# Kernel tuning notes

Measured on AMD Instinct MI355X. Metric: run time of the kernel, lower is better.

Reference implementation:

```python
import jax, jax.numpy as jnp
import numpy as np
import math

BS, LQ, LKV = 4, 2048, 2048
D_LATENT, D_MODEL, HEADS = 512, 512, 8
D_K = D_MODEL // HEADS


def setup_inputs() -> dict:
    key = jax.random.key(0)
    ks = jax.random.split(key, 12)
    s = 0.02
    return {
        "q": jax.random.normal(ks[0], (BS, LQ, D_LATENT), jnp.float32),
        "k": jax.random.normal(ks[1], (BS, LKV, D_MODEL), jnp.float32),
        "v": jax.random.normal(ks[2], (BS, LKV, D_MODEL), jnp.float32),
        "weights": jax.random.uniform(ks[3], (BS, LKV), jnp.float32) + 1e-3,
        "Wq": jax.random.normal(ks[4], (D_LATENT, D_MODEL), jnp.float32) * s,
        "bq": jnp.zeros((D_MODEL,), jnp.float32),
        "Wk": jax.random.normal(ks[5], (D_MODEL, D_MODEL), jnp.float32) * s,
        "bk": jnp.zeros((D_MODEL,), jnp.float32),
        "Wv": jax.random.normal(ks[6], (D_MODEL, D_MODEL), jnp.float32) * s,
        "bv": jnp.zeros((D_MODEL,), jnp.float32),
        "Wo": jax.random.normal(ks[7], (D_MODEL, D_MODEL), jnp.float32) * s,
        "bo": jnp.zeros((D_MODEL,), jnp.float32),
    }


def reference(q, k, v, weights, Wq, bq, Wk, bk, Wv, bv, Wo, bo):
    bs = q.shape[0]
    # QKV projections, split into heads: [bs, h, L, d_k]
    qh = (q @ Wq + bq).reshape(bs, -1, HEADS, D_K).transpose(0, 2, 1, 3)
    kh = (k @ Wk + bk).reshape(bs, -1, HEADS, D_K).transpose(0, 2, 1, 3)
    vh = (v @ Wv + bv).reshape(bs, -1, HEADS, D_K).transpose(0, 2, 1, 3)
    # scaled dot-product scores [bs, h, Lq, Lkv]
    scores = jnp.einsum("bhqd,bhkd->bhqk", qh, kh) / math.sqrt(D_K)
    p = jax.nn.softmax(scores, axis=-1)
    # post-softmax external weight renormalization
    wp = p * weights[:, None, None, :]
    wp = wp / wp.sum(-1, keepdims=True)
    out = jnp.einsum("bhqk,bhkd->bhqd", wp, vh)
    concat = out.transpose(0, 2, 1, 3).reshape(bs, -1, D_MODEL)
    return concat @ Wo + bo
```

## Files before the change

### kernel.cpp

```cpp
#include <hip/hip_runtime.h>
#include <hip/hip_bf16.h>

#define LQ 2048
#define LKV 2048
#define DM 512
#define NH 8
#define DK 64

typedef __attribute__((ext_vector_type(8))) __bf16 bf16x8;
typedef __attribute__((ext_vector_type(4))) float f32x4;
typedef __attribute__((ext_vector_type(16))) float f32x16;

#define AS1 __attribute__((address_space(1)))
#define AS3 __attribute__((address_space(3)))

static __device__ __forceinline__ unsigned short f2bf(float x) {
  unsigned u = __float_as_uint(x);
  return (unsigned short)((u + 0x7fffu + ((u >> 16) & 1u)) >> 16);
}
static __device__ __forceinline__ float bf2f(unsigned short u) {
  return __uint_as_float(((unsigned)u) << 16);
}
static __device__ __forceinline__ bf16x8 cvt8(f32x4 a, f32x4 b) {
  bf16x8 r;
  r[0] = (__bf16)a[0]; r[1] = (__bf16)a[1]; r[2] = (__bf16)a[2]; r[3] = (__bf16)a[3];
  r[4] = (__bf16)b[0]; r[5] = (__bf16)b[1]; r[6] = (__bf16)b[2]; r[7] = (__bf16)b[3];
  return r;
}

__global__ __launch_bounds__(256) void transpose_w(
    const float* __restrict__ Wq, const float* __restrict__ Wk,
    const float* __restrict__ Wv, const float* __restrict__ Wo,
    const float* __restrict__ wts,
    unsigned short* __restrict__ WtAll, unsigned short* __restrict__ wbf)
{
  const float* W = blockIdx.z == 0 ? Wq : blockIdx.z == 1 ? Wk : blockIdx.z == 2 ? Wv : Wo;
  unsigned short* Wt = WtAll + (size_t)blockIdx.z * DM * DM;
  __shared__ float tile[32][33];
  const int t = threadIdx.x;
  if (blockIdx.z == 0 && blockIdx.y == 0) {
    int idx = blockIdx.x * 512 + t * 2;
#pragma unroll
    for (int i = 0; i < 2; ++i) {
      int kv = idx + i;
      int r = kv & 15;
      int ph = (r & 3) | ((r & 4) << 1) | ((r & 8) >> 1);
      wbf[(kv & ~15) | ph] = f2bf(wts[kv]);
    }
  }
  const int tr = t >> 3;
  const int tc4 = (t & 7) * 4;
  const int k0 = blockIdx.x * 32, n0 = blockIdx.y * 32;
  float4 v = *(const float4*)(W + (size_t)(k0 + tr) * DM + n0 + tc4);
  tile[tr][tc4 + 0] = v.x; tile[tr][tc4 + 1] = v.y;
  tile[tr][tc4 + 2] = v.z; tile[tr][tc4 + 3] = v.w;
  __syncthreads();
  ushort4 o;
  o.x = f2bf(tile[tc4 + 0][tr]);
  o.y = f2bf(tile[tc4 + 1][tr]);
  o.z = f2bf(tile[tc4 + 2][tr]);
  o.w = f2bf(tile[tc4 + 3][tr]);
  *(ushort4*)(Wt + (size_t)(n0 + tr) * DM + k0 + tc4) = o;
}

__global__ __launch_bounds__(256) void gemm_qkv(
    const float* __restrict__ qin, const float* __restrict__ kin, const float* __restrict__ vin,
    const unsigned short* __restrict__ WtAll,
    const float* __restrict__ bq, const float* __restrict__ bk, const float* __restrict__ bv,
    unsigned short* __restrict__ qh, unsigned short* __restrict__ kh, unsigned short* __restrict__ vh)
{
  const int bid = blockIdx.x;
  const int x = bid & 7, j = bid >> 3;
  const int p = x + 8 * (j >> 2);
  const int nt = j & 3;
  const int mode = p >> 6, mtile = p & 63;

  const float* A = mode == 0 ? qin : (mode == 1 ? kin : vin);
  const unsigned short* Bt = WtAll + (size_t)mode * DM * DM;
  const float* bias = mode == 0 ? bq : (mode == 1 ? bk : bv);
  unsigned short* out = mode == 0 ? qh : (mode == 1 ? kh : vh);
  const float scale = (mode == 0) ? 0.18033688011112042f : 1.0f;

  __shared__ __align__(16) float As[128 * 32];
  __shared__ __align__(16) unsigned short Bs[128 * 32];

  const int tid = threadIdx.x;
  const int lane = tid & 63;
  const int w = tid >> 6;
  const int wr = w >> 1, wc = w & 1;
  const int l15 = lane & 15, g = lane >> 4;
  const int m0 = mtile * 128, n0 = nt * 128;

  f32x4 acc[4][4] = {};

  for (int k0 = 0; k0 < DM; k0 += 32) {
#pragma unroll
    for (int i = 0; i < 4; ++i) {
      int c = tid + i * 256;
      int row = c >> 3, slot = c & 7;
      const float* src = A + (size_t)(m0 + row) * DM + k0 + ((slot ^ (row & 7)) << 2);
      __builtin_amdgcn_global_load_lds((const AS1 unsigned*)src,
                                       (AS3 unsigned*)((char*)As + c * 16), 16, 0, 0);
    }
#pragma unroll
    for (int i = 0; i < 2; ++i) {
      int c = tid + i * 256;
      int row = c >> 2, slot = c & 3;
      const unsigned short* src = Bt + (size_t)(n0 + row) * DM + k0 + ((slot ^ ((row >> 1) & 3)) * 8);
      __builtin_amdgcn_global_load_lds((const AS1 unsigned*)src,
                                       (AS3 unsigned*)((char*)Bs + c * 16), 16, 0, 0);
    }
    __syncthreads();

    bf16x8 af[4], bfr[4];
#pragma unroll
    for (int mi = 0; mi < 4; ++mi) {
      int row = wr * 64 + mi * 16 + l15;
      f32x4 a0 = *(const f32x4*)((const char*)As + row * 128 + (((2 * g) ^ (row & 7)) << 4));
      f32x4 a1 = *(const f32x4*)((const char*)As + row * 128 + (((2 * g + 1) ^ (row & 7)) << 4));
      af[mi] = cvt8(a0, a1);
    }
#pragma unroll
    for (int ni = 0; ni < 4; ++ni) {
      int row = wc * 64 + ni * 16 + l15;
      bfr[ni] = *(const bf16x8*)((const char*)Bs + row * 64 + ((g ^ ((row >> 1) & 3)) * 16));
    }
#pragma unroll
    for (int mi = 0; mi < 4; ++mi)
#pragma unroll
      for (int ni = 0; ni < 4; ++ni)
        acc[mi][ni] = __builtin_amdgcn_mfma_f32_16x16x32_bf16(af[mi], bfr[ni], acc[mi][ni], 0, 0, 0);
    __syncthreads();
  }

#pragma unroll
  for (int mi = 0; mi < 4; ++mi) {
#pragma unroll
    for (int ni = 0; ni < 4; ++ni) {
      int n = n0 + wc * 64 + ni * 16 + l15;
      float bs = bias[n];
      int h = n >> 6, d = n & 63;
#pragma unroll
      for (int r = 0; r < 4; ++r) {
        int m = m0 + wr * 64 + mi * 16 + g * 4 + r;
        int b = m >> 11, li = m & 2047;
        float val = (acc[mi][ni][r] + bs) * scale;
        out[(((size_t)(b * NH + h)) * LQ + li) * DK + d] = f2bf(val);
      }
    }
  }
}

__global__ __launch_bounds__(256) void gemm_out(
    const unsigned short* __restrict__ A, const unsigned short* __restrict__ Bt,
    const float* __restrict__ bias, float* __restrict__ out)
{
  __shared__ __align__(16) unsigned short Al[128 * 32];
  __shared__ __align__(16) unsigned short Bl[128 * 32];
  const int tid = threadIdx.x;
  const int lane = tid & 63;
  const int w = tid >> 6;
  const int wr = w >> 1, wc = w & 1;
  const int l15 = lane & 15, g = lane >> 4;
  const int m0 = blockIdx.x * 128, n0 = blockIdx.y * 128;
  f32x4 acc[4][4] = {};

  for (int k0 = 0; k0 < DM; k0 += 32) {
#pragma unroll
    for (int i = 0; i < 2; ++i) {
      int c = tid + i * 256;
      int row = c >> 2, slot = c & 3;
      int so = (slot ^ ((row >> 1) & 3)) * 8;
      __builtin_amdgcn_global_load_lds(
          (const AS1 unsigned*)(A + (size_t)(m0 + row) * DM + k0 + so),
          (AS3 unsigned*)((char*)Al + c * 16), 16, 0, 0);
      __builtin_amdgcn_global_load_lds(
          (const AS1 unsigned*)(Bt + (size_t)(n0 + row) * DM + k0 + so),
          (AS3 unsigned*)((char*)Bl + c * 16), 16, 0, 0);
    }
    __syncthreads();
    bf16x8 af[4], bfr[4];
#pragma unroll
    for (int mi = 0; mi < 4; ++mi) {
      int row = wr * 64 + mi * 16 + l15;
      af[mi] = *(const bf16x8*)((const char*)Al + row * 64 + ((g ^ ((row >> 1) & 3)) * 16));
    }
#pragma unroll
    for (int ni = 0; ni < 4; ++ni) {
      int row = wc * 64 + ni * 16 + l15;
      bfr[ni] = *(const bf16x8*)((const char*)Bl + row * 64 + ((g ^ ((row >> 1) & 3)) * 16));
    }
#pragma unroll
    for (int mi = 0; mi < 4; ++mi)
#pragma unroll
      for (int ni = 0; ni < 4; ++ni)
        acc[mi][ni] = __builtin_amdgcn_mfma_f32_16x16x32_bf16(af[mi], bfr[ni], acc[mi][ni], 0, 0, 0);
    __syncthreads();
  }

#pragma unroll
  for (int mi = 0; mi < 4; ++mi) {
#pragma unroll
    for (int ni = 0; ni < 4; ++ni) {
      int n = n0 + wc * 64 + ni * 16 + l15;
      float bs = bias[n];
#pragma unroll
      for (int r = 0; r < 4; ++r) {
        int m = m0 + wr * 64 + mi * 16 + g * 4 + r;
        out[(size_t)m * DM + n] = acc[mi][ni][r] + bs;
      }
    }
  }
}

__global__ __launch_bounds__(256) void prep_kv(
    const unsigned short* __restrict__ kh, const unsigned short* __restrict__ vh,
    const float* __restrict__ wts,
    unsigned short* __restrict__ kf, unsigned short* __restrict__ vf)
{
  __shared__ __align__(16) unsigned short t[64 * 72];
  const int bh = blockIdx.y, l0 = blockIdx.x * 64;
  const int b = bh >> 3;
  const size_t base = (size_t)bh * LKV * DK;
  const int tid = threadIdx.x;

#pragma unroll
  for (int i = 0; i < 2; ++i) {
    int c = tid + i * 256;
    int sl = c & 63, cq = (c >> 6) & 3, tl = c >> 8;
    int kv = tl * 32 + (sl & 31);
    int4 blk = *(const int4*)(kh + base + (size_t)(l0 + kv) * DK + cq * 16 + (sl >> 5) * 8);
    *(int4*)(kf + base + ((((size_t)(l0 >> 5) + tl) * 4 + cq) * 64 + sl) * 8) = blk;
  }

#pragma unroll
  for (int i = 0; i < 2; ++i) {
    int idx = tid + i * 256;
    int row = idx >> 3, seg = idx & 7;
    *(int4*)(&t[row * 72 + seg * 8]) =
        *(const int4*)(vh + base + (size_t)(l0 + row) * DK + seg * 8);
  }
  __syncthreads();
#pragma unroll
  for (int i = 0; i < 2; ++i) {
    int idx = tid + i * 256;
    int d = idx >> 3, seg = idx & 7;
    int kvg = l0 + seg * 8;
    float4 wa = *(const float4*)(wts + b * LKV + kvg);
    float4 wb4 = *(const float4*)(wts + b * LKV + kvg + 4);
    unsigned short r0 = f2bf(wa.x * bf2f(t[(seg * 8 + 0) * 72 + d]));
    unsigned short r1 = f2bf(wa.y * bf2f(t[(seg * 8 + 1) * 72 + d]));
    unsigned short r2 = f2bf(wa.z * bf2f(t[(seg * 8 + 2) * 72 + d]));
    unsigned short r3 = f2bf(wa.w * bf2f(t[(seg * 8 + 3) * 72 + d]));
    unsigned short r4 = f2bf(wb4.x * bf2f(t[(seg * 8 + 4) * 72 + d]));
    unsigned short r5 = f2bf(wb4.y * bf2f(t[(seg * 8 + 5) * 72 + d]));
    unsigned short r6 = f2bf(wb4.z * bf2f(t[(seg * 8 + 6) * 72 + d]));
    unsigned short r7 = f2bf(wb4.w * bf2f(t[(seg * 8 + 7) * 72 + d]));
    int T = kvg >> 4, s = (kvg >> 3) & 1, dh = d >> 5, dl = d & 31;
    size_t slot = (((size_t)bh * 128 + T) * 2 + dh) * 64;
    ushort4 lo4, hi4;
    lo4.x = r0; lo4.y = r1; lo4.z = r2; lo4.w = r3;
    hi4.x = r4; hi4.y = r5; hi4.z = r6; hi4.w = r7;
    *(ushort4*)(vf + (slot + dl) * 8 + 4 * s) = lo4;
    *(ushort4*)(vf + (slot + dl + 32) * 8 + 4 * s) = hi4;
  }
}

__global__ __launch_bounds__(512, 4) void attn_fwd(
    const unsigned short* __restrict__ qh, const unsigned short* __restrict__ kf,
    const unsigned short* __restrict__ vf, const unsigned short* __restrict__ wbf,
    unsigned short* __restrict__ ao)
{
  const int bid = blockIdx.x;
  const int xcd = bid & 7, wi = bid >> 3;
  const int bh = xcd * 4 + (wi >> 4);
  const int qb = wi & 15;
  const int b = bh >> 3, h = bh & 7;
  const int tid = threadIdx.x, lane = tid & 63, w = tid >> 6;
  const int wq = w & 3, half = w >> 2;
  const int l31 = lane & 31, hi = lane >> 5;

  __shared__ __align__(16) char smem[36928];

  const size_t kv_bh = (size_t)bh * (LKV * DK);
  const unsigned short* kfb = kf + kv_bh;
  const unsigned short* vfb = vf + kv_bh;

  const int q0 = qb * 128 + wq * 32;

#define STAGE(buf, t)                                                                     \
  do {                                                                                    \
    int tg_ = half * 32 + (t);                                                            \
    const unsigned short* ks_ = kfb + ((size_t)(tg_ * 4 + wq) * 64 + lane) * 8;           \
    const unsigned short* vs_ = vfb + ((size_t)((tg_ * 2 + (wq >> 1)) * 2 + (wq & 1)) * 64 + lane) * 8; \
    char* kd_ = smem + (buf) * 16384 + half * 8192 + wq * 1024;                           \
    char* vd_ = smem + (buf) * 16384 + half * 8192 + 4096 + wq * 1024;                    \
    __builtin_amdgcn_global_load_lds((const AS1 unsigned*)ks_, (AS3 unsigned*)kd_, 16, 0, 0); \
    __builtin_amdgcn_global_load_lds((const AS1 unsigned*)vs_, (AS3 unsigned*)vd_, 16, 0, 0); \
  } while (0)

  if (tid < 256)
    __builtin_amdgcn_global_load_lds((const AS1 unsigned*)(wbf + b * LKV + tid * 8),
                                     (AS3 unsigned*)(smem + 32768 + tid * 16), 16, 0, 0);
  if (tid < 16) *(int*)(smem + 36864 + tid * 4) = 0;
  STAGE(0, 0);

  bf16x8 qf[4];
  {
    const unsigned short* qp = qh + kv_bh + (size_t)(q0 + l31) * DK + hi * 8;
#pragma unroll
    for (int cq = 0; cq < 4; ++cq) qf[cq] = *(const bf16x8*)(qp + cq * 16);
  }
  __syncthreads();

  const char* wl = smem + 32768 + half * 2048 + hi * 16;
  const char* zpad = smem + 36864;
  f32x16 accO0 = {}, accO1 = {}, accL = {};
  int cur = 0;

#pragma unroll 2
  for (int t = 0; t < 32; ++t) {
    if (t < 31) {
      STAGE(cur ^ 1, t + 1);
      asm volatile("s_waitcnt vmcnt(2)" ::: "memory");
    } else {
      asm volatile("s_waitcnt vmcnt(0)" ::: "memory");
    }
    __builtin_amdgcn_s_barrier();

    const char* Kb = smem + cur * 16384 + half * 8192;
    const char* Vb = Kb + 4096;

    __builtin_amdgcn_s_setprio(1);
    f32x16 s = {};
#pragma unroll
    for (int cq = 0; cq < 4; ++cq) {
      bf16x8 kfr = *(const bf16x8*)(Kb + cq * 1024 + lane * 16);
      s = __builtin_amdgcn_mfma_f32_32x32x16_bf16(kfr, qf[cq], s, 0, 0, 0);
    }

    union { unsigned u[8]; bf16x8 v[2]; } P;
#pragma unroll
    for (int r2 = 0; r2 < 8; ++r2) {
      float lo = __builtin_amdgcn_exp2f(s[2 * r2]);
      float hv = __builtin_amdgcn_exp2f(s[2 * r2 + 1]);
      __bf16 bl = (__bf16)lo, bh2 = (__bf16)hv;
      unsigned short ul = __builtin_bit_cast(unsigned short, bl);
      unsigned short uh = __builtin_bit_cast(unsigned short, bh2);
      P.u[r2] = (unsigned)ul | ((unsigned)uh << 16);
    }

    const char* wsel = (l31 == 0) ? (wl + t * 64) : zpad;

#pragma unroll
    for (int c = 0; c < 2; ++c) {
      bf16x8 vb0 = *(const bf16x8*)(Vb + (c * 2 + 0) * 1024 + lane * 16);
      bf16x8 vb1 = *(const bf16x8*)(Vb + (c * 2 + 1) * 1024 + lane * 16);
      bf16x8 wb = *(const bf16x8*)(wsel + c * 32);

      accO0 = __builtin_amdgcn_mfma_f32_32x32x16_bf16(P.v[c], vb0, accO0, 0, 0, 0);
      accO1 = __builtin_amdgcn_mfma_f32_32x32x16_bf16(P.v[c], vb1, accO1, 0, 0, 0);
      accL  = __builtin_amdgcn_mfma_f32_32x32x16_bf16(P.v[c], wb,  accL,  0, 0, 0);
    }
    __builtin_amdgcn_s_setprio(0);

    asm volatile("s_waitcnt lgkmcnt(0)" ::: "memory");
    __builtin_amdgcn_s_barrier();
    cur ^= 1;
  }
#undef STAGE

  float* Ob = (float*)smem;
  float* Lb = (float*)(smem + 34816);
  if (half == 1) {
#pragma unroll
    for (int r = 0; r < 16; ++r) {
      int qp_ = (r & 3) + 8 * (r >> 2) + 4 * hi;
      Ob[(wq * 32 + qp_) * 68 + l31] = accO0[r];
      Ob[(wq * 32 + qp_) * 68 + 32 + l31] = accO1[r];
    }
    if (l31 == 0) {
#pragma unroll
      for (int r = 0; r < 16; ++r) {
        int qp_ = (r & 3) + 8 * (r >> 2) + 4 * hi;
        Lb[wq * 32 + qp_] = accL[r];
      }
    }
  }
  __syncthreads();
  if (half == 0) {
#pragma unroll
    for (int r = 0; r < 16; ++r) {
      int qp_ = (r & 3) + 8 * (r >> 2) + 4 * hi;
      float L = __shfl(accL[r], lane & 32) + Lb[wq * 32 + qp_];
      float inv = 1.0f / L;
      float o0 = accO0[r] + Ob[(wq * 32 + qp_) * 68 + l31];
      float o1 = accO1[r] + Ob[(wq * 32 + qp_) * 68 + 32 + l31];
      size_t off = ((size_t)(b * LQ + q0 + qp_)) * DM + h * DK;
      ao[off + l31] = f2bf(o0 * inv);
      ao[off + 32 + l31] = f2bf(o1 * inv);
    }
  }
}

extern "C" void kernel_launch(void* const* d_in, const int* in_sizes, int n_in,
                              void* d_out, int out_size, void* d_ws, size_t ws_size,
                              hipStream_t stream)
{
  const float* q  = (const float*)d_in[0];
  const float* k  = (const float*)d_in[1];
  const float* v  = (const float*)d_in[2];
  const float* wt = (const float*)d_in[3];
  const float* Wq = (const float*)d_in[4];
  const float* bq = (const float*)d_in[5];
  const float* Wk = (const float*)d_in[6];
  const float* bk = (const float*)d_in[7];
  const float* Wv = (const float*)d_in[8];
  const float* bv = (const float*)d_in[9];
  const float* Wo = (const float*)d_in[10];
  const float* bo = (const float*)d_in[11];

  char* ws = (char*)d_ws;
  unsigned short* qh = (unsigned short*)(ws + 0);
  unsigned short* kfr= (unsigned short*)(ws + 8388608);
  unsigned short* vfr= (unsigned short*)(ws + 16777216);
  unsigned short* ao = (unsigned short*)(ws + 25165824);
  unsigned short* Wt = (unsigned short*)(ws + 33554432);
  unsigned short* vh = (unsigned short*)(ws + 35651584);
  unsigned short* wbf= (unsigned short*)(ws + 44040192);
  unsigned short* kh = ao;

  transpose_w<<<dim3(16, 16, 4), 256, 0, stream>>>(Wq, Wk, Wv, Wo, wt, Wt, wbf);
  gemm_qkv<<<768, 256, 0, stream>>>(q, k, v, Wt, bq, bk, bv, qh, kh, vh);
  prep_kv<<<dim3(32, 32), 256, 0, stream>>>(kh, vh, wt, kfr, vfr);
  attn_fwd<<<512, 512, 0, stream>>>(qh, kfr, vfr, wbf, ao);
  gemm_out<<<dim3(64, 4), 256, 0, stream>>>(ao, Wt + 3 * (size_t)DM * DM, bo, (float*)d_out);
}
```

Baseline: 92.98 us.

## Double-buffer projection GEMMs and drop K reformatting pass in prep kernel

Both projection GEMMs now use two LDS buffers, issuing the next K-slice's global-to-LDS loads before computing the current one. Explicit vmcnt waits, raw barriers and setprio replace __syncthreads. Separately, the K copy in the prep kernel is removed and attention reads K straight from the head-major layout using the same per-lane addressing. This cuts one read and one write pass over K, but gemm_qkv's LDS use doubles to 48KB, which may lower occupancy.

```diff
diff --git a/kernel.cpp b/kernel.cpp
--- a/kernel.cpp
+++ b/kernel.cpp
@@ -81,8 +81,7 @@
   unsigned short* out = mode == 0 ? qh : (mode == 1 ? kh : vh);
   const float scale = (mode == 0) ? 0.18033688011112042f : 1.0f;
 
-  __shared__ __align__(16) float As[128 * 32];
-  __shared__ __align__(16) unsigned short Bs[128 * 32];
+  __shared__ __align__(16) char sm[49152];
 
   const int tid = threadIdx.x;
   const int lane = tid & 63;
@@ -91,47 +90,71 @@
   const int l15 = lane & 15, g = lane >> 4;
   const int m0 = mtile * 128, n0 = nt * 128;
 
+#define STAGEQ(buf, t)                                                                    \
+  do {                                                                                    \
+    int k0_ = (t) * 32;                                                                   \
+    char* As_ = sm + (buf) * 24576;                                                       \
+    char* Bs_ = As_ + 16384;                                                              \
+    _Pragma("unroll")                                                                     \
+    for (int i = 0; i < 4; ++i) {                                                         \
+      int c = tid + i * 256;                                                              \
+      int row = c >> 3, slot = c & 7;                                                     \
+      const float* src = A + (size_t)(m0 + row) * DM + k0_ + ((slot ^ (row & 7)) << 2);   \
+      __builtin_amdgcn_global_load_lds((const AS1 unsigned*)src,                          \
+                                       (AS3 unsigned*)(As_ + c * 16), 16, 0, 0);          \
+    }                                                                                     \
+    _Pragma("unroll")                                                                     \
+    for (int i = 0; i < 2; ++i) {                                                         \
+      int c = tid + i * 256;                                                              \
+      int row = c >> 2, slot = c & 3;                                                     \
+      const unsigned short* src = Bt + (size_t)(n0 + row) * DM + k0_ + ((slot ^ ((row >> 1) & 3)) * 8); \
+      __builtin_amdgcn_global_load_lds((const AS1 unsigned*)src,                          \
+                                       (AS3 unsigned*)(Bs_ + c * 16), 16, 0, 0);          \
+    }                                                                                     \
+  } while (0)
+
   f32x4 acc[4][4] = {};
-
-  for (int k0 = 0; k0 < DM; k0 += 32) {
-#pragma unroll
-    for (int i = 0; i < 4; ++i) {
-      int c = tid + i * 256;
-      int row = c >> 3, slot = c & 7;
-      const float* src = A + (size_t)(m0 + row) * DM + k0 + ((slot ^ (row & 7)) << 2);
-      __builtin_amdgcn_global_load_lds((const AS1 unsigned*)src,
-                                       (AS3 unsigned*)((char*)As + c * 16), 16, 0, 0);
-    }
-#pragma unroll
-    for (int i = 0; i < 2; ++i) {
-      int c = tid + i * 256;
-      int row = c >> 2, slot = c & 3;
-      const unsigned short* src = Bt + (size_t)(n0 + row) * DM + k0 + ((slot ^ ((row >> 1) & 3)) * 8);
-      __builtin_amdgcn_global_load_lds((const AS1 unsigned*)src,
-                                       (AS3 unsigned*)((char*)Bs + c * 16), 16, 0, 0);
-    }
-    __syncthreads();
-
+  STAGEQ(0, 0);
+  int cur = 0;
+
+  for (int t = 0; t < 16; ++t) {
+    if (t < 15) {
+      STAGEQ(cur ^ 1, t + 1);
+      asm volatile("s_waitcnt vmcnt(6)" ::: "memory");
+    } else {
+      asm volatile("s_waitcnt vmcnt(0)" ::: "memory");
+    }
+    __builtin_amdgcn_s_barrier();
+
+    const char* As_ = sm + cur * 24576;
+    const char* Bs_ = As_ + 16384;
+
+    __builtin_amdgcn_s_setprio(1);
     bf16x8 af[4], bfr[4];
 #pragma unroll
     for (int mi = 0; mi < 4; ++mi) {
       int row = wr * 64 + mi * 16 + l15;
-      f32x4 a0 = *(const f32x4*)((const char*)As + row * 128 + (((2 * g) ^ (row & 7)) << 4));
-      f32x4 a1 = *(const f32x4*)((const char*)As + row * 128 + (((2 * g + 1) ^ (row & 7)) << 4));
+      f32x4 a0 = *(const f32x4*)(As_ + row * 128 + (((2 * g) ^ (row & 7)) << 4));
+      f32x4 a1 = *(const f32x4*)(As_ + row * 128 + (((2 * g + 1) ^ (row & 7)) << 4));
       af[mi] = cvt8(a0, a1);
     }
 #pragma unroll
     for (int ni = 0; ni < 4; ++ni) {
       int row = wc * 64 + ni * 16 + l15;
-      bfr[ni] = *(const bf16x8*)((const char*)Bs + row * 64 + ((g ^ ((row >> 1) & 3)) * 16));
+      bfr[ni] = *(const bf16x8*)(Bs_ + row * 64 + ((g ^ ((row >> 1) & 3)) * 16));
     }
 #pragma unroll
     for (int mi = 0; mi < 4; ++mi)
 #pragma unroll
       for (int ni = 0; ni < 4; ++ni)
         acc[mi][ni] = __builtin_amdgcn_mfma_f32_16x16x32_bf16(af[mi], bfr[ni], acc[mi][ni], 0, 0, 0);
-    __syncthreads();
-  }
+    __builtin_amdgcn_s_setprio(0);
+
+    asm volatile("s_waitcnt lgkmcnt(0)" ::: "memory");
+    __builtin_amdgcn_s_barrier();
+    cur ^= 1;
+  }
+#undef STAGEQ
 
 #pragma unroll
   for (int mi = 0; mi < 4; ++mi) {
@@ -155,48 +178,73 @@
     const unsigned short* __restrict__ A, const unsigned short* __restrict__ Bt,
     const float* __restrict__ bias, float* __restrict__ out)
 {
-  __shared__ __align__(16) unsigned short Al[128 * 32];
-  __shared__ __align__(16) unsigned short Bl[128 * 32];
+  __shared__ __align__(16) char sm[32768];
   const int tid = threadIdx.x;
   const int lane = tid & 63;
   const int w = tid >> 6;
   const int wr = w >> 1, wc = w & 1;
   const int l15 = lane & 15, g = lane >> 4;
   const int m0 = blockIdx.x * 128, n0 = blockIdx.y * 128;
+
+#define STAGEO(buf, t)                                                                    \
+  do {                                                                                    \
+    int k0_ = (t) * 32;                                                                   \
+    char* Al_ = sm + (buf) * 16384;                                                       \
+    char* Bl_ = Al_ + 8192;                                                               \
+    _Pragma("unroll")                                                                     \
+    for (int i = 0; i < 2; ++i) {                                                         \
+      int c = tid + i * 256;                                                              \
+      int row = c >> 2, slot = c & 3;                                                     \
+      int so = (slot ^ ((row >> 1) & 3)) * 8;                                             \
+      __builtin_amdgcn_global_load_lds(                                                   \
+          (const AS1 unsigned*)(A + (size_t)(m0 + row) * DM + k0_ + so),                  \
+          (AS3 unsigned*)(Al_ + c * 16), 16, 0, 0);                                       \
+      __builtin_amdgcn_global_load_lds(                                                   \
+          (const AS1 unsigned*)(Bt + (size_t)(n0 + row) * DM + k0_ + so),                 \
+          (AS3 unsigned*)(Bl_ + c * 16), 16, 0, 0);                                       \
+    }                                                                                     \
+  } while (0)
+
   f32x4 acc[4][4] = {};
-
-  for (int k0 = 0; k0 < DM; k0 += 32) {
-#pragma unroll
-    for (int i = 0; i < 2; ++i) {
-      int c = tid + i * 256;
-      int row = c >> 2, slot = c & 3;
-      int so = (slot ^ ((row >> 1) & 3)) * 8;
-      __builtin_amdgcn_global_load_lds(
-          (const AS1 unsigned*)(A + (size_t)(m0 + row) * DM + k0 + so),
-          (AS3 unsigned*)((char*)Al + c * 16), 16, 0, 0);
-      __builtin_amdgcn_global_load_lds(
-          (const AS1 unsigned*)(Bt + (size_t)(n0 + row) * DM + k0 + so),
-          (AS3 unsigned*)((char*)Bl + c * 16), 16, 0, 0);
-    }
-    __syncthreads();
+  STAGEO(0, 0);
+  int cur = 0;
+
+  for (int t = 0; t < 16; ++t) {
+    if (t < 15) {
+      STAGEO(cur ^ 1, t + 1);
+      asm volatile("s_waitcnt vmcnt(4)" ::: "memory");
+    } else {
+      asm volatile("s_waitcnt vmcnt(0)" ::: "memory");
+    }
+    __builtin_amdgcn_s_barrier();
+
+    const char* Al_ = sm + cur * 16384;
+    const char* Bl_ = Al_ + 8192;
+
+    __builtin_amdgcn_s_setprio(1);
     bf16x8 af[4], bfr[4];
 #pragma unroll
     for (int mi = 0; mi < 4; ++mi) {
       int row = wr * 64 + mi * 16 + l15;
-      af[mi] = *(const bf16x8*)((const char*)Al + row * 64 + ((g ^ ((row >> 1) & 3)) * 16));
+      af[mi] = *(const bf16x8*)(Al_ + row * 64 + ((g ^ ((row >> 1) & 3)) * 16));
     }
 #pragma unroll
     for (int ni = 0; ni < 4; ++ni) {
       int row = wc * 64 + ni * 16 + l15;
-      bfr[ni] = *(const bf16x8*)((const char*)Bl + row * 64 + ((g ^ ((row >> 1) & 3)) * 16));
+      bfr[ni] = *(const bf16x8*)(Bl_ + row * 64 + ((g ^ ((row >> 1) & 3)) * 16));
     }
 #pragma unroll
     for (int mi = 0; mi < 4; ++mi)
 #pragma unroll
       for (int ni = 0; ni < 4; ++ni)
         acc[mi][ni] = __builtin_amdgcn_mfma_f32_16x16x32_bf16(af[mi], bfr[ni], acc[mi][ni], 0, 0, 0);
-    __syncthreads();
-  }
+    __builtin_amdgcn_s_setprio(0);
+
+    asm volatile("s_waitcnt lgkmcnt(0)" ::: "memory");
+    __builtin_amdgcn_s_barrier();
+    cur ^= 1;
+  }
+#undef STAGEO
 
 #pragma unroll
   for (int mi = 0; mi < 4; ++mi) {
@@ -213,25 +261,15 @@
   }
 }
 
-__global__ __launch_bounds__(256) void prep_kv(
-    const unsigned short* __restrict__ kh, const unsigned short* __restrict__ vh,
-    const float* __restrict__ wts,
-    unsigned short* __restrict__ kf, unsigned short* __restrict__ vf)
+__global__ __launch_bounds__(256) void prep_v(
+    const unsigned short* __restrict__ vh, const float* __restrict__ wts,
+    unsigned short* __restrict__ vf)
 {
   __shared__ __align__(16) unsigned short t[64 * 72];
   const int bh = blockIdx.y, l0 = blockIdx.x * 64;
   const int b = bh >> 3;
   const size_t base = (size_t)bh * LKV * DK;
   const int tid = threadIdx.x;
-
-#pragma unroll
-  for (int i = 0; i < 2; ++i) {
-    int c = tid + i * 256;
-    int sl = c & 63, cq = (c >> 6) & 3, tl = c >> 8;
-    int kv = tl * 32 + (sl & 31);
-    int4 blk = *(const int4*)(kh + base + (size_t)(l0 + kv) * DK + cq * 16 + (sl >> 5) * 8);
-    *(int4*)(kf + base + ((((size_t)(l0 >> 5) + tl) * 4 + cq) * 64 + sl) * 8) = blk;
-  }
 
 #pragma unroll
   for (int i = 0; i < 2; ++i) {
@@ -267,7 +305,7 @@
 }
 
 __global__ __launch_bounds__(512, 4) void attn_fwd(
-    const unsigned short* __restrict__ qh, const unsigned short* __restrict__ kf,
+    const unsigned short* __restrict__ qh, const unsigned short* __restrict__ kh,
     const unsigned short* __restrict__ vf, const unsigned short* __restrict__ wbf,
     unsigned short* __restrict__ ao)
 {
@@ -283,7 +321,7 @@
   __shared__ __align__(16) char smem[36928];
 
   const size_t kv_bh = (size_t)bh * (LKV * DK);
-  const unsigned short* kfb = kf + kv_bh;
+  const unsigned short* khb = kh + kv_bh;
   const unsigned short* vfb = vf + kv_bh;
 
   const int q0 = qb * 128 + wq * 32;
@@ -291,7 +329,8 @@
 #define STAGE(buf, t)                                                                     \
   do {                                                                                    \
     int tg_ = half * 32 + (t);                                                            \
-    const unsigned short* ks_ = kfb + ((size_t)(tg_ * 4 + wq) * 64 + lane) * 8;           \
+    int kv_ = tg_ * 32 + (lane & 31);                                                     \
+    const unsigned short* ks_ = khb + (size_t)kv_ * DK + wq * 16 + (lane >> 5) * 8;       \
     const unsigned short* vs_ = vfb + ((size_t)((tg_ * 2 + (wq >> 1)) * 2 + (wq & 1)) * 64 + lane) * 8; \
     char* kd_ = smem + (buf) * 16384 + half * 8192 + wq * 1024;                           \
     char* vd_ = smem + (buf) * 16384 + half * 8192 + 4096 + wq * 1024;                    \
@@ -422,17 +461,16 @@
 
   char* ws = (char*)d_ws;
   unsigned short* qh = (unsigned short*)(ws + 0);
-  unsigned short* kfr= (unsigned short*)(ws + 8388608);
+  unsigned short* kh = (unsigned short*)(ws + 8388608);
   unsigned short* vfr= (unsigned short*)(ws + 16777216);
   unsigned short* ao = (unsigned short*)(ws + 25165824);
   unsigned short* Wt = (unsigned short*)(ws + 33554432);
   unsigned short* vh = (unsigned short*)(ws + 35651584);
   unsigned short* wbf= (unsigned short*)(ws + 44040192);
-  unsigned short* kh = ao;
 
   transpose_w<<<dim3(16, 16, 4), 256, 0, stream>>>(Wq, Wk, Wv, Wo, wt, Wt, wbf);
   gemm_qkv<<<768, 256, 0, stream>>>(q, k, v, Wt, bq, bk, bv, qh, kh, vh);
-  prep_kv<<<dim3(32, 32), 256, 0, stream>>>(kh, vh, wt, kfr, vfr);
-  attn_fwd<<<512, 512, 0, stream>>>(qh, kfr, vfr, wbf, ao);
+  prep_v<<<dim3(32, 32), 256, 0, stream>>>(vh, wt, vfr);
+  attn_fwd<<<512, 512, 0, stream>>>(qh, kh, vfr, wbf, ao);
   gemm_out<<<dim3(64, 4), 256, 0, stream>>>(ao, Wt + 3 * (size_t)DM * DM, bo, (float*)d_out);
 }
```

New measurement: 89.17 us. -4.1%, faster.
